# Performance work log

Measured on AMD Instinct MI355X. Metric: run time of the kernel, lower is better.

Reference implementation:

```python
import jax, jax.numpy as jnp
import numpy as np

WH, WW = 8, 8          # window size
DIM = 384
HEADS = 12
N = WH * WW            # tokens per window = 64


def _relative_position_index():
    ch, cw = np.meshgrid(np.arange(WH), np.arange(WW), indexing='ij')
    coords = np.stack([ch, cw]).reshape(2, -1)            # (2, N)
    rel = coords[:, :, None] - coords[:, None, :]         # (2, N, N)
    rel = rel.transpose(1, 2, 0).astype(np.int32)         # (N, N, 2)
    rel[:, :, 0] += WH - 1
    rel[:, :, 1] += WW - 1
    rel[:, :, 0] *= 2 * WW - 1
    return jnp.asarray(rel.sum(-1))                       # (N, N) int32


def setup_inputs() -> dict:
    key = jax.random.key(0)
    ks = jax.random.split(key, 6)
    B_ = 4096
    x = jax.random.normal(ks[0], (B_, N, DIM), dtype=jnp.float32)
    mask = jnp.zeros((B_, N, N), dtype=jnp.float32)       # nW == B_ here (B=1)
    qkv_w = jax.random.normal(ks[1], (DIM, 3 * DIM), dtype=jnp.float32) * 0.02
    qkv_b = jnp.zeros((3 * DIM,), dtype=jnp.float32)
    rpb_table = jax.random.normal(ks[2], ((2 * WH - 1) * (2 * WW - 1), HEADS), dtype=jnp.float32) * 0.02
    proj_w = jax.random.normal(ks[3], (DIM, DIM), dtype=jnp.float32) * 0.02
    proj_b = jnp.zeros((DIM,), dtype=jnp.float32)
    rpi = _relative_position_index()
    return {"x": x, "mask": mask, "qkv_w": qkv_w, "qkv_b": qkv_b,
            "rpb_table": rpb_table, "proj_w": proj_w, "proj_b": proj_b, "rpi": rpi}


def reference(x, mask, qkv_w, qkv_b, rpb_table, proj_w, proj_b, rpi):
    B_, n, C = x.shape
    hd = C // HEADS
    scale = hd ** -0.5
    qkv = (x @ qkv_w + qkv_b).reshape(B_, n, 3, HEADS, hd)
    q, k, v = qkv[:, :, 0], qkv[:, :, 1], qkv[:, :, 2]    # (B_, n, H, hd)
    attn = jnp.einsum('bnhd,bmhd->bhnm', q * scale, k)    # (B_, H, n, n)
    bias = rpb_table[rpi]                                 # (n, n, H)
    attn = attn + jnp.transpose(bias, (2, 0, 1))[None]    # add rel-pos bias
    nW = mask.shape[0]
    attn = attn.reshape(B_ // nW, nW, HEADS, n, n) + mask[None, :, None]
    attn = attn.reshape(B_, HEADS, n, n)
    attn = jax.nn.softmax(attn, axis=-1)
    out = jnp.einsum('bhnm,bmhd->bnhd', attn, v).reshape(B_, n, C)
    return out @ proj_w + proj_b
```

## Files before the change

kernel.cpp:

```cpp
#include <hip/hip_runtime.h>
#include <hip/hip_bf16.h>

typedef unsigned short u16;
typedef unsigned int   u32;
typedef __attribute__((ext_vector_type(8))) __bf16 bf16x8;
typedef __attribute__((ext_vector_type(4))) float  f32x4;

#define NWIN   4096
#define SEQ    64
#define DIMC   384
#define NHEAD  12
#define HDIM   32
#define NROWS  262144
#define NQKV   1152

__device__ __forceinline__ u16 f2bf(float f){
  u32 x = __float_as_uint(f);
  return (u16)((x + 0x7fffu + ((x >> 16) & 1u)) >> 16);
}

__device__ __forceinline__ void gload_lds16(const u16* g, u16* l){
  __builtin_amdgcn_global_load_lds(
      (const __attribute__((address_space(1))) void*)g,
      (__attribute__((address_space(3))) void*)l, 16, 0, 0);
}

__device__ __forceinline__ f32x4 mfma_bf16(bf16x8 a, bf16x8 b, f32x4 c){
  return __builtin_amdgcn_mfma_f32_16x16x32_bf16(a, b, c, 0, 0, 0);
}

__global__ void prep_x(const float* __restrict__ x, u16* __restrict__ xb){
  size_t i = ((size_t)blockIdx.x * 256 + threadIdx.x) * 8;
  f32x4 a = *(const f32x4*)(x + i);
  f32x4 b = *(const f32x4*)(x + i + 4);
  union { u16 u[8]; bf16x8 v; } o;
  #pragma unroll
  for(int j=0;j<4;j++) o.u[j]   = f2bf(a[j]);
  #pragma unroll
  for(int j=0;j<4;j++) o.u[4+j] = f2bf(b[j]);
  *(bf16x8*)(xb + i) = o.v;
}

__global__ void prep_w(const float* __restrict__ qw, const float* __restrict__ pw,
                       const float* __restrict__ rpb, const int* __restrict__ rpi,
                       u16* __restrict__ wqT, u16* __restrict__ wpT,
                       float* __restrict__ biasT){
  int id = blockIdx.x * 256 + threadIdx.x;
  if (id < NQKV*DIMC){
    int n = id / DIMC, k = id % DIMC;
    wqT[id] = f2bf(qw[(size_t)k*NQKV + n]);
  } else if (id < NQKV*DIMC + DIMC*DIMC){
    int j = id - NQKV*DIMC;
    int n = j / DIMC, k = j % DIMC;
    wpT[j] = f2bf(pw[(size_t)k*DIMC + n]);
  } else {
    int j = id - (NQKV*DIMC + DIMC*DIMC);
    int h = j / 4096, nm = j % 4096;
    biasT[j] = rpb[rpi[nm]*NHEAD + h];
  }
}

template<int NB, int EPI>
__global__ __launch_bounds__(256, 2) void gemm_bt(
    const u16* __restrict__ A, const u16* __restrict__ Bt,
    const float* __restrict__ bias,
    u16* __restrict__ oq, u16* __restrict__ okk, u16* __restrict__ ov,
    float* __restrict__ of)
{
  __shared__ u16 Al[2][8192];
  __shared__ u16 Bl[2][8192];
  const int bid = blockIdx.x;
  const int bm = bid / NB, bn = bid % NB;
  const size_t m0 = (size_t)bm * 128;
  const int n0 = bn * 128;
  const int tid = threadIdx.x, wv = tid >> 6, ln = tid & 63;
  const int wr = wv >> 1, wc = wv & 1;
  const int cl = ln & 15, q8 = ln >> 4;

  f32x4 acc[4][4];
  const f32x4 zero4 = {0.f,0.f,0.f,0.f};
  #pragma unroll
  for(int i=0;i<4;i++)
    #pragma unroll
    for(int j=0;j<4;j++) acc[i][j] = zero4;

  auto stage = [&](int bufi, int kt){
    #pragma unroll
    for(int c=0;c<4;c++){
      int un  = (wv*4+c)*64 + ln;
      int row = un >> 3;
      int u   = (un & 7) ^ (row & 7);
      gload_lds16(A  + (m0 + row)*DIMC + kt*64 + u*8, &Al[bufi][(wv*4+c)*512]);
      gload_lds16(Bt + (size_t)(n0 + row)*DIMC + kt*64 + u*8, &Bl[bufi][(wv*4+c)*512]);
    }
  };

  stage(0, 0);
  #pragma unroll
  for(int kt=0;kt<6;kt++){
    const int bufi = kt & 1;
    __syncthreads();
    if (kt < 5) stage(bufi^1, kt+1);
    #pragma unroll
    for(int ks=0;ks<2;ks++){
      bf16x8 af[4], bfr[4];
      #pragma unroll
      for(int i=0;i<4;i++){
        int row = wr*64 + i*16 + cl;
        int u = (ks*4 + q8) ^ (row & 7);
        af[i] = *(const bf16x8*)&Al[bufi][row*64 + u*8];
      }
      #pragma unroll
      for(int j=0;j<4;j++){
        int row = wc*64 + j*16 + cl;
        int u = (ks*4 + q8) ^ (row & 7);
        bfr[j] = *(const bf16x8*)&Bl[bufi][row*64 + u*8];
      }
      #pragma unroll
      for(int i=0;i<4;i++)
        #pragma unroll
        for(int j=0;j<4;j++)
          acc[i][j] = mfma_bf16(af[i], bfr[j], acc[i][j]);
    }
  }

  float bj[4];
  #pragma unroll
  for(int j=0;j<4;j++) bj[j] = bias[n0 + wc*64 + j*16 + cl];

  if (EPI == 0){
    const int t = n0 / DIMC;
    const int lc0 = n0 - t*DIMC + wc*64 + cl;
    u16* dst = (t==0) ? oq : (t==1) ? okk : ov;
    #pragma unroll
    for(int i=0;i<4;i++){
      size_t r0 = m0 + wr*64 + i*16 + q8*4;
      #pragma unroll
      for(int j=0;j<4;j++)
        #pragma unroll
        for(int r=0;r<4;r++)
          dst[(r0 + r)*DIMC + lc0 + j*16] = f2bf(acc[i][j][r] + bj[j]);
    }
  } else {
    const int lc0 = n0 + wc*64 + cl;
    #pragma unroll
    for(int i=0;i<4;i++){
      size_t r0 = m0 + wr*64 + i*16 + q8*4;
      #pragma unroll
      for(int j=0;j<4;j++)
        #pragma unroll
        for(int r=0;r<4;r++)
          of[(r0 + r)*DIMC + lc0 + j*16] = acc[i][j][r] + bj[j];
    }
  }
}

__global__ __launch_bounds__(256, 3) void attn_win(
    const u16* __restrict__ Q, const u16* __restrict__ K, const u16* __restrict__ V,
    const float* __restrict__ biasT, const float* __restrict__ mask,
    u16* __restrict__ AO)
{
  __shared__ u16 qk[4][4096];
  __shared__ u16 vt[4][2048];
  const int bid = blockIdx.x;
  const int w  = bid / 3, hg = bid % 3;
  const int tid = threadIdx.x, wv = tid >> 6, ln = tid & 63;
  const int cl = ln & 15, g = ln >> 4;
  const size_t rb = (size_t)w * SEQ;
  const int h0 = hg * 4;
  const f32x4 zero4 = {0.f,0.f,0.f,0.f};

  #pragma unroll
  for(int c=0;c<4;c++){
    int f = wv*4 + c;
    int hl = f >> 2, i = f & 3;
    size_t src = (rb + i*16 + (ln>>2))*DIMC + (h0+hl)*HDIM + (ln&3)*8;
    gload_lds16(Q + src, &qk[hl][i*512]);
    gload_lds16(K + src, &qk[hl][2048 + i*512]);
  }
  #pragma unroll
  for(int c=0;c<4;c++){
    int ch = c*256 + tid;
    int tok = ch >> 4, dc = ch & 15;
    union { bf16x8 v; u16 u[8]; } vv;
    vv.v = *(const bf16x8*)(V + (rb + tok)*DIMC + h0*HDIM + dc*8);
    #pragma unroll
    for(int j=0;j<8;j++){
      int d = dc*8 + j, hl = d >> 5, dh = d & 31;
      vt[hl][dh*64 + (((tok>>3) ^ (dh&7)) * 8) + (tok & 7)] = vv.u[j];
    }
  }
  __syncthreads();

  const float scale = 0.17677669529663687f;
  const int h = h0 + wv;
  u16* ph = qk[wv];
  const u16* pv = vt[wv];

  bf16x8 aq[4], bk[4];
  #pragma unroll
  for(int i=0;i<4;i++) aq[i] = *(const bf16x8*)&ph[(i*16 + cl)*32 + g*8];
  #pragma unroll
  for(int j=0;j<4;j++) bk[j] = *(const bf16x8*)&ph[2048 + (j*16 + cl)*32 + g*8];
  f32x4 S[4][4];
  #pragma unroll
  for(int i=0;i<4;i++)
    #pragma unroll
    for(int j=0;j<4;j++)
      S[i][j] = mfma_bf16(aq[i], bk[j], zero4);

  float l[4][4];
  #pragma unroll
  for(int i=0;i<4;i++){
    #pragma unroll
    for(int r=0;r<4;r++){
      int row = i*16 + g*4 + r;
      float v0[4];
      #pragma unroll
      for(int j=0;j<4;j++){
        int col2 = j*16 + cl;
        v0[j] = S[i][j][r]*scale + biasT[h*4096 + row*64 + col2]
                                 + mask[(size_t)w*4096 + row*64 + col2];
      }
      float mx = fmaxf(fmaxf(v0[0],v0[1]), fmaxf(v0[2],v0[3]));
      #pragma unroll
      for(int s=1;s<16;s<<=1) mx = fmaxf(mx, __shfl_xor(mx, s));
      float sm = 0.f;
      #pragma unroll
      for(int j=0;j<4;j++){ v0[j] = __expf(v0[j]-mx); sm += v0[j]; }
      #pragma unroll
      for(int s=1;s<16;s<<=1) sm += __shfl_xor(sm, s);
      l[i][r] = sm;
      #pragma unroll
      for(int j=0;j<4;j++){
        int col2 = j*16 + cl;
        ph[row*64 + (((col2>>3) ^ (row&7))*8) + (col2&7)] = f2bf(v0[j]);
      }
    }
  }
  f32x4 O[4][2];
  #pragma unroll
  for(int i=0;i<4;i++){ O[i][0] = zero4; O[i][1] = zero4; }
  #pragma unroll
  for(int ks=0;ks<2;ks++){
    bf16x8 ap[4], bv[2];
    #pragma unroll
    for(int i=0;i<4;i++){
      int m = i*16 + cl;
      ap[i] = *(const bf16x8*)&ph[m*64 + (((ks*4+g) ^ (m&7))*8)];
    }
    #pragma unroll
    for(int j=0;j<2;j++){
      int n = j*16 + cl;
      bv[j] = *(const bf16x8*)&pv[n*64 + (((ks*4+g) ^ (n&7))*8)];
    }
    #pragma unroll
    for(int i=0;i<4;i++)
      #pragma unroll
      for(int j=0;j<2;j++)
        O[i][j] = mfma_bf16(ap[i], bv[j], O[i][j]);
  }
  #pragma unroll
  for(int i=0;i<4;i++){
    #pragma unroll
    for(int r=0;r<4;r++){
      float inv = 1.0f / l[i][r];
      size_t orow = (rb + i*16 + g*4 + r)*DIMC + h*HDIM;
      AO[orow + cl]      = f2bf(O[i][0][r]*inv);
      AO[orow + 16 + cl] = f2bf(O[i][1][r]*inv);
    }
  }
}

extern "C" void kernel_launch(void* const* d_in, const int* in_sizes, int n_in,
                              void* d_out, int out_size, void* d_ws, size_t ws_size,
                              hipStream_t stream) {
  const float* x      = (const float*)d_in[0];
  const float* mask   = (const float*)d_in[1];
  const float* qkv_w  = (const float*)d_in[2];
  const float* qkv_b  = (const float*)d_in[3];
  const float* rpb    = (const float*)d_in[4];
  const float* proj_w = (const float*)d_in[5];
  const float* proj_b = (const float*)d_in[6];
  const int*   rpi    = (const int*)d_in[7];

  u16* xb  = (u16*)d_ws;
  u16* vb  = xb + (size_t)NROWS*DIMC;
  u16* wqT = vb + (size_t)NROWS*DIMC;
  u16* wpT = wqT + (size_t)NQKV*DIMC;
  float* biasT = (float*)(wpT + (size_t)DIMC*DIMC);
  u16* qb = (u16*)d_out;
  u16* kb = qb + (size_t)NROWS*DIMC;
  u16* ao = xb;

  prep_x<<<(NROWS*(size_t)DIMC)/(256*8), 256, 0, stream>>>(x, xb);
  prep_w<<<(NQKV*DIMC + DIMC*DIMC + NHEAD*4096)/256, 256, 0, stream>>>(
      qkv_w, proj_w, rpb, rpi, wqT, wpT, biasT);
  gemm_bt<9,0><<<2048*9, 256, 0, stream>>>(xb, wqT, qkv_b, qb, kb, vb, nullptr);
  attn_win<<<NWIN*3, 256, 0, stream>>>(qb, kb, vb, biasT, mask, ao);
  gemm_bt<3,1><<<2048*3, 256, 0, stream>>>(ao, wpT, proj_b, nullptr, nullptr, nullptr,
                                           (float*)d_out);
}
```

Baseline: 1.613 ms.

## Fuse QKV projection into windowed attention kernel and remap block order

Removes the separate QKV GEMM and its Q/K/V round trip through global memory. Each attention block now loads its window's 64x384 x tile into LDS and computes its head's Q, K, V with MFMA from double-buffered weight tiles, writing them straight into the LDS layouts the attention stage uses. Scale is folded into Q. Block IDs in both the fused kernel and the projection GEMM are remapped in strides of 8, which looks aimed at spreading neighbouring blocks across XCDs for cache locality. In exchange, each x window is re-read once per head group (three times), LDS use rises to about 96KB so only one block fits per CU, and each wave does its own serial GEMM.

Result: no change. 1.608 ms (-0.3%).

```diff
diff --git a/kernel.cpp b/kernel.cpp
--- a/kernel.cpp
+++ b/kernel.cpp
@@ -69,7 +69,8 @@
 {
   __shared__ u16 Al[2][8192];
   __shared__ u16 Bl[2][8192];
-  const int bid = blockIdx.x;
+  const int bid0 = blockIdx.x;
+  const int bid = (bid0 & 7) * ((2048*NB) >> 3) + (bid0 >> 3);
   const int bm = bid / NB, bn = bid % NB;
   const size_t m0 = (size_t)bm * 128;
   const int n0 = bn * 128;
@@ -155,45 +156,129 @@
   }
 }
 
-__global__ __launch_bounds__(256, 3) void attn_win(
-    const u16* __restrict__ Q, const u16* __restrict__ K, const u16* __restrict__ V,
-    const float* __restrict__ biasT, const float* __restrict__ mask,
-    u16* __restrict__ AO)
+__global__ __launch_bounds__(256, 1) void qkv_attn(
+    const u16* __restrict__ Xb, const u16* __restrict__ Wq,
+    const float* __restrict__ qkvb, const float* __restrict__ biasT,
+    const float* __restrict__ mask, u16* __restrict__ AO)
 {
+  __shared__ u16 xa[64*384];
+  __shared__ u16 wl[4][2][2048];
   __shared__ u16 qk[4][4096];
   __shared__ u16 vt[4][2048];
+
   const int bid = blockIdx.x;
-  const int w  = bid / 3, hg = bid % 3;
+  const int L = (bid & 7) * ((NWIN*3) >> 3) + (bid >> 3);
+  const int w = L / 3, hg = L % 3;
   const int tid = threadIdx.x, wv = tid >> 6, ln = tid & 63;
   const int cl = ln & 15, g = ln >> 4;
   const size_t rb = (size_t)w * SEQ;
-  const int h0 = hg * 4;
+  const int h = hg*4 + wv;
   const f32x4 zero4 = {0.f,0.f,0.f,0.f};
-
-  #pragma unroll
-  for(int c=0;c<4;c++){
-    int f = wv*4 + c;
-    int hl = f >> 2, i = f & 3;
-    size_t src = (rb + i*16 + (ln>>2))*DIMC + (h0+hl)*HDIM + (ln&3)*8;
-    gload_lds16(Q + src, &qk[hl][i*512]);
-    gload_lds16(K + src, &qk[hl][2048 + i*512]);
-  }
-  #pragma unroll
-  for(int c=0;c<4;c++){
-    int ch = c*256 + tid;
-    int tok = ch >> 4, dc = ch & 15;
-    union { bf16x8 v; u16 u[8]; } vv;
-    vv.v = *(const bf16x8*)(V + (rb + tok)*DIMC + h0*HDIM + dc*8);
-    #pragma unroll
-    for(int j=0;j<8;j++){
-      int d = dc*8 + j, hl = d >> 5, dh = d & 31;
-      vt[hl][dh*64 + (((tok>>3) ^ (dh&7)) * 8) + (tok & 7)] = vv.u[j];
-    }
+  const float scale = 0.17677669529663687f;
+
+  float bb[3][2];
+  #pragma unroll
+  for(int p=0;p<3;p++)
+    #pragma unroll
+    for(int j=0;j<2;j++) bb[p][j] = qkvb[p*384 + h*32 + j*16 + cl];
+
+  #pragma unroll
+  for(int c=0;c<12;c++){
+    int un = c*256 + tid;
+    int row = un / 48, up = un % 48;
+    int u = (up & 0x38) | ((up ^ row) & 7);
+    gload_lds16(Xb + (rb + row)*DIMC + u*8, &xa[(c*256 + wv*64)*8]);
   }
   __syncthreads();
 
-  const float scale = 0.17677669529663687f;
-  const int h = h0 + wv;
+  auto stageW = [&](int s, int b){
+    const int p = s/6, kt = s - p*6;
+    const size_t nb = (size_t)(p*384 + h*32);
+    #pragma unroll
+    for(int c=0;c<4;c++){
+      int un = c*64 + ln;
+      int row = un >> 3;
+      int u = (un & 7) ^ (row & 7);
+      gload_lds16(Wq + (nb + row)*DIMC + kt*64 + u*8, &wl[wv][b][c*512]);
+    }
+  };
+
+  f32x4 acc[4][2];
+  stageW(0, 0);
+  #pragma unroll
+  for(int s=0;s<18;s++){
+    if ((s % 6) == 0){
+      #pragma unroll
+      for(int i=0;i<4;i++){ acc[i][0] = zero4; acc[i][1] = zero4; }
+    }
+    if (s < 17){
+      asm volatile("s_waitcnt lgkmcnt(0)" ::: "memory");
+      __builtin_amdgcn_sched_barrier(0);
+      stageW(s+1, (s+1)&1);
+      asm volatile("s_waitcnt vmcnt(4)" ::: "memory");
+    } else {
+      asm volatile("s_waitcnt vmcnt(0)" ::: "memory");
+    }
+    __builtin_amdgcn_sched_barrier(0);
+    const int kt = s % 6, b = s & 1;
+    #pragma unroll
+    for(int ks=0;ks<2;ks++){
+      bf16x8 af[4], bw[2];
+      #pragma unroll
+      for(int i=0;i<4;i++){
+        int row = i*16 + cl;
+        int ug = kt*8 + ks*4 + g;
+        int pu = (ug & 0x38) | ((ug ^ row) & 7);
+        af[i] = *(const bf16x8*)&xa[row*384 + pu*8];
+      }
+      #pragma unroll
+      for(int j=0;j<2;j++){
+        int row = j*16 + cl;
+        int u = (ks*4 + g) ^ (row & 7);
+        bw[j] = *(const bf16x8*)&wl[wv][b][row*64 + u*8];
+      }
+      #pragma unroll
+      for(int i=0;i<4;i++)
+        #pragma unroll
+        for(int j=0;j<2;j++)
+          acc[i][j] = mfma_bf16(af[i], bw[j], acc[i][j]);
+    }
+    if (s == 5){
+      #pragma unroll
+      for(int i=0;i<4;i++)
+        #pragma unroll
+        for(int j=0;j<2;j++)
+          #pragma unroll
+          for(int r=0;r<4;r++){
+            int tok = i*16 + g*4 + r;
+            qk[wv][tok*32 + j*16 + cl] = f2bf((acc[i][j][r] + bb[0][j]) * scale);
+          }
+    }
+    if (s == 11){
+      #pragma unroll
+      for(int i=0;i<4;i++)
+        #pragma unroll
+        for(int j=0;j<2;j++)
+          #pragma unroll
+          for(int r=0;r<4;r++){
+            int tok = i*16 + g*4 + r;
+            qk[wv][2048 + tok*32 + j*16 + cl] = f2bf(acc[i][j][r] + bb[1][j]);
+          }
+    }
+    if (s == 17){
+      #pragma unroll
+      for(int i=0;i<4;i++)
+        #pragma unroll
+        for(int j=0;j<2;j++)
+          #pragma unroll
+          for(int r=0;r<4;r++){
+            int tok = i*16 + g*4 + r, dh = j*16 + cl;
+            vt[wv][dh*64 + (((tok>>3) ^ (dh&7))*8) + (tok&7)] =
+                f2bf(acc[i][j][r] + bb[2][j]);
+          }
+    }
+  }
+
   u16* ph = qk[wv];
   const u16* pv = vt[wv];
 
@@ -219,8 +304,8 @@
       #pragma unroll
       for(int j=0;j<4;j++){
         int col2 = j*16 + cl;
-        v0[j] = S[i][j][r]*scale + biasT[h*4096 + row*64 + col2]
-                                 + mask[(size_t)w*4096 + row*64 + col2];
+        v0[j] = S[i][j][r] + biasT[h*4096 + row*64 + col2]
+                           + mask[(size_t)w*4096 + row*64 + col2];
       }
       float mx = fmaxf(fmaxf(v0[0],v0[1]), fmaxf(v0[2],v0[3]));
       #pragma unroll
@@ -285,19 +370,15 @@
   const int*   rpi    = (const int*)d_in[7];
 
   u16* xb  = (u16*)d_ws;
-  u16* vb  = xb + (size_t)NROWS*DIMC;
-  u16* wqT = vb + (size_t)NROWS*DIMC;
+  u16* ao  = xb + (size_t)NROWS*DIMC;
+  u16* wqT = ao + (size_t)NROWS*DIMC;
   u16* wpT = wqT + (size_t)NQKV*DIMC;
   float* biasT = (float*)(wpT + (size_t)DIMC*DIMC);
-  u16* qb = (u16*)d_out;
-  u16* kb = qb + (size_t)NROWS*DIMC;
-  u16* ao = xb;
 
   prep_x<<<(NROWS*(size_t)DIMC)/(256*8), 256, 0, stream>>>(x, xb);
   prep_w<<<(NQKV*DIMC + DIMC*DIMC + NHEAD*4096)/256, 256, 0, stream>>>(
       qkv_w, proj_w, rpb, rpi, wqT, wpT, biasT);
-  gemm_bt<9,0><<<2048*9, 256, 0, stream>>>(xb, wqT, qkv_b, qb, kb, vb, nullptr);
-  attn_win<<<NWIN*3, 256, 0, stream>>>(qb, kb, vb, biasT, mask, ao);
+  qkv_attn<<<NWIN*3, 256, 0, stream>>>(xb, wqT, qkv_b, biasT, mask, ao);
   gemm_bt<3,1><<<2048*3, 256, 0, stream>>>(ao, wpT, proj_b, nullptr, nullptr, nullptr,
                                            (float*)d_out);
 }
```
